# Kernel tuning notes

Hardware: AMD Instinct MI355X
Metric: run time of the kernel (lower is better)

## Reference

```python
import jax, jax.numpy as jnp
import numpy as np

# DeformConv3d hyperparams (from init_kwargs)
STRIDE = (1, 1, 1)
PAD = (1, 1, 1)
DIL = (1, 1, 1)
GROUPS = 1
DEFORM_GROUPS = 1  # reference assumes dg == 1


def setup_inputs() -> dict:
    key = jax.random.key(0)
    k1, k2, k3, k4 = jax.random.split(key, 4)
    x = jax.random.normal(k1, (2, 32, 24, 24, 24), jnp.float32)
    # offset channels = 3 * dg * kD*kH*kW = 81, layout [k_idx, (dz,dy,dx)]
    offset = jax.random.normal(k2, (2, 81, 24, 24, 24), jnp.float32)
    weight = jax.random.normal(k3, (64, 32, 3, 3, 3), jnp.float32) * 0.05
    bias = jax.random.normal(k4, (64,), jnp.float32) * 0.05
    return {"x": x, "offset": offset, "weight": weight, "bias": bias}


def _deform_conv3d(x, offset, weight, bias):
    B, C, D, H, W = x.shape
    Cout, Cg, kD, kH, kW = weight.shape
    sD, sH, sW = STRIDE
    pD, pH, pW = PAD
    dD, dH, dW = DIL
    Kn = kD * kH * kW
    Do = (D + 2 * pD - dD * (kD - 1) - 1) // sD + 1
    Ho = (H + 2 * pH - dH * (kH - 1) - 1) // sH + 1
    Wo = (W + 2 * pW - dW * (kW - 1) - 1) // sW + 1
    N = Do * Ho * Wo

    # offset: [B, Kn*3, Do,Ho,Wo] -> [B, Kn, 3, N]
    off = offset.reshape(B, Kn, 3, N)

    # kernel tap grid [Kn]
    kz, ky, kx = jnp.meshgrid(jnp.arange(kD), jnp.arange(kH), jnp.arange(kW), indexing='ij')
    kz, ky, kx = kz.reshape(Kn), ky.reshape(Kn), kx.reshape(Kn)
    # output grid [N]
    oz, oy, ox = jnp.meshgrid(jnp.arange(Do), jnp.arange(Ho), jnp.arange(Wo), indexing='ij')
    oz, oy, ox = oz.reshape(N), oy.reshape(N), ox.reshape(N)

    # sampling coords [B, Kn, N]
    z = (oz[None, None, :] * sD - pD) + kz[None, :, None] * dD + off[:, :, 0]
    y = (oy[None, None, :] * sH - pH) + ky[None, :, None] * dH + off[:, :, 1]
    xx = (ox[None, None, :] * sW - pW) + kx[None, :, None] * dW + off[:, :, 2]

    z0 = jnp.floor(z); fz = z - z0
    y0 = jnp.floor(y); fy = y - y0
    x0 = jnp.floor(xx); fx = xx - x0

    x_flat = x.reshape(B, C, D * H * W)
    acc = jnp.zeros((B, C, Kn * N), x.dtype)
    # 8 trilinear corners (fixed small loop)
    for dz in (0, 1):
        iz = z0 + dz
        wz = fz if dz else (1.0 - fz)
        for dy in (0, 1):
            iy = y0 + dy
            wy = fy if dy else (1.0 - fy)
            for dx in (0, 1):
                ix = x0 + dx
                wx = fx if dx else (1.0 - fx)
                valid = ((iz >= 0) & (iz < D) & (iy >= 0) & (iy < H)
                         & (ix >= 0) & (ix < W))
                w = (wz * wy * wx) * valid.astype(x.dtype)  # [B,Kn,N]
                izc = jnp.clip(iz, 0, D - 1).astype(jnp.int32)
                iyc = jnp.clip(iy, 0, H - 1).astype(jnp.int32)
                ixc = jnp.clip(ix, 0, W - 1).astype(jnp.int32)
                idx = (izc * H + iyc) * W + ixc  # [B,Kn,N]
                g = jnp.take_along_axis(x_flat, idx.reshape(B, 1, Kn * N), axis=2)
                acc = acc + g * w.reshape(B, 1, Kn * N)

    # im2col columns ordered (c, kz, ky, kx) to match weight layout
    cols = acc.reshape(B, C * Kn, N)
    Cpg = C // GROUPS
    Opg = Cout // GROUPS
    cols_g = cols.reshape(B, GROUPS, Cpg * Kn, N)
    w_g = weight.reshape(GROUPS, Opg, Cpg * Kn)
    out = jnp.einsum('gok,bgkn->bgon', w_g, cols_g).reshape(B, Cout, N)
    out = out + bias[None, :, None]
    return out.reshape(B, Cout, Do, Ho, Wo)


def reference(x, offset, weight, bias):
    return _deform_conv3d(x, offset, weight, bias)
```

## Files before the change

kernel.cpp:

```cpp
#include <hip/hip_runtime.h>
#include <hip/hip_fp16.h>


constexpr int B   = 2;
constexpr int C   = 32;
constexpr int D   = 24, H = 24, W = 24;
constexpr int CO  = 64;
constexpr int KN  = 27;
constexpr int DHW = D * H * W;
constexpr int N   = DHW;
constexpr int CK  = C * KN;

constexpr int TPB_MAIN = 256;
constexpr int NBLK     = (B * N) / 64;

constexpr int PREPX_BLKS = (B * DHW) / 256;
constexpr int PREPW_BLKS = (CO * CK) / 256;

using h8v   = __attribute__((ext_vector_type(8))) _Float16;
using f32x4 = __attribute__((ext_vector_type(4))) float;

__device__ __forceinline__ h8v splat8(float w) {
    const _Float16 h = (_Float16)w;
    h8v r;
    #pragma unroll
    for (int i = 0; i < 8; ++i) r[i] = h;
    return r;
}

__device__ __forceinline__ unsigned pack2h(float a, float b) {
    const _Float16 ha = (_Float16)a, hb = (_Float16)b;
    unsigned short ua, ub;
    __builtin_memcpy(&ua, &ha, 2);
    __builtin_memcpy(&ub, &hb, 2);
    return (unsigned)ua | ((unsigned)ub << 16);
}

__global__ __launch_bounds__(256)
void prep_fused(const float* __restrict__ x, const float* __restrict__ wgt,
                _Float16* __restrict__ xT, _Float16* __restrict__ wp) {
    const int bid = blockIdx.x;
    if (bid < PREPX_BLKS) {
        __shared__ unsigned s_t[256 * 21];
        const int tid = threadIdx.x;
        const int v0  = bid * 256;
        const int b   = (v0 >= DHW) ? 1 : 0;
        const int vox = (v0 - b * DHW) + tid;
        const float* xb = x + (size_t)(b * C) * DHW + vox;
        #pragma unroll
        for (int c2 = 0; c2 < 16; ++c2) {
            const float f0 = xb[(size_t)(2 * c2)     * DHW];
            const float f1 = xb[(size_t)(2 * c2 + 1) * DHW];
            s_t[tid * 21 + c2] = pack2h(f0, f1);
        }
        __syncthreads();
        unsigned r[16];
        #pragma unroll
        for (int j = 0; j < 16; ++j) r[j] = s_t[tid * 21 + j];
        int4* dst = reinterpret_cast<int4*>(xT + ((size_t)(v0 + tid)) * 32);
        dst[0] = make_int4(r[0],  r[1],  r[2],  r[3]);
        dst[1] = make_int4(r[4],  r[5],  r[6],  r[7]);
        dst[2] = make_int4(r[8],  r[9],  r[10], r[11]);
        dst[3] = make_int4(r[12], r[13], r[14], r[15]);
    } else {
        const int idx   = (bid - PREPX_BLKS) * 256 + threadIdx.x;
        const int j     = idx & 7;
        const int lane  = (idx >> 3) & 63;
        const int t     = idx >> 9;
        const int otile = t / 27;
        const int kstep = t - otile * 27;
        const int o     = otile * 16 + (lane & 15);
        const int c     = 8 * (lane >> 4) + j;
        wp[idx] = (_Float16)wgt[(size_t)o * CK + c * KN + kstep];
    }
}

__global__ __launch_bounds__(TPB_MAIN)
void deform_main(const float* __restrict__ off,
                 const _Float16* __restrict__ xT,
                 const _Float16* __restrict__ wp,
                 const float* __restrict__ bias,
                 float* __restrict__ out) {
    const int tid  = threadIdx.x;
    const int lane = tid & 63;
    const int wv   = tid >> 6;
    const int p    = lane & 15;
    const int q    = lane >> 4;

    const int gp = blockIdx.x * 64 + wv * 16 + p;
    const int b  = (gp >= N) ? 1 : 0;
    const int n  = gp - b * N;
    const int oz = n / 576;
    const int rr = n - oz * 576;
    const int oy = rr / 24;
    const int ox = rr - oy * 24;

    const float* offb  = off + (size_t)(b * 81) * N + n;
    const h8v*   xbase = reinterpret_cast<const h8v*>(xT) + (size_t)b * DHW * 4;
    const h8v*   wbase = reinterpret_cast<const h8v*>(wp);

    f32x4 acc[4];
    #pragma unroll
    for (int ot = 0; ot < 4; ++ot) acc[ot] = (f32x4){0.f, 0.f, 0.f, 0.f};

    #pragma unroll 1
    for (int ks = 0; ks < KN; ++ks) {
        const int kz = ks / 9;
        const int kr = ks - kz * 9;
        const int ky = kr / 3;
        const int kx = kr - ky * 3;

        const float offz = offb[(size_t)(ks * 3 + 0) * N];
        const float offy = offb[(size_t)(ks * 3 + 1) * N];
        const float offx = offb[(size_t)(ks * 3 + 2) * N];

        h8v afr[4];
        #pragma unroll
        for (int ot = 0; ot < 4; ++ot)
            afr[ot] = wbase[(ot * 27 + ks) * 64 + lane];

        const float z  = (float)(oz - 1 + kz) + offz;
        const float y  = (float)(oy - 1 + ky) + offy;
        const float xx = (float)(ox - 1 + kx) + offx;
        const float zf = floorf(z), yf = floorf(y), xf = floorf(xx);
        const float fz = z - zf, fy = y - yf, fx = xx - xf;
        const int z0 = (int)zf, y0 = (int)yf, x0 = (int)xf;

        int   cidx[8];
        float cw[8];
        #pragma unroll
        for (int cr = 0; cr < 8; ++cr) {
            const int cz = cr >> 2, cy = (cr >> 1) & 1, cx = cr & 1;
            const int iz = z0 + cz, iy = y0 + cy, ix = x0 + cx;
            const bool vd = ((unsigned)iz < (unsigned)D) &&
                            ((unsigned)iy < (unsigned)H) &&
                            ((unsigned)ix < (unsigned)W);
            const int izc = min(max(iz, 0), D - 1);
            const int iyc = min(max(iy, 0), H - 1);
            const int ixc = min(max(ix, 0), W - 1);
            cidx[cr] = (izc * H + iyc) * W + ixc;
            const float wz = cz ? fz : 1.0f - fz;
            const float wy = cy ? fy : 1.0f - fy;
            const float wx = cx ? fx : 1.0f - fx;
            cw[cr] = vd ? (wz * wy * wx) : 0.0f;
        }

        h8v v[8];
        #pragma unroll
        for (int cr = 0; cr < 8; ++cr)
            v[cr] = xbase[(size_t)cidx[cr] * 4 + q];

        h8v bfr = splat8(0.0f);
        #pragma unroll
        for (int cr = 0; cr < 8; ++cr)
            bfr += v[cr] * splat8(cw[cr]);

        #pragma unroll
        for (int ot = 0; ot < 4; ++ot)
            acc[ot] = __builtin_amdgcn_mfma_f32_16x16x32_f16(afr[ot], bfr,
                                                             acc[ot], 0, 0, 0);
    }

    #pragma unroll
    for (int ot = 0; ot < 4; ++ot) {
        #pragma unroll
        for (int r = 0; r < 4; ++r) {
            const int o = ot * 16 + q * 4 + r;
            out[((size_t)(b * CO + o)) * N + n] = acc[ot][r] + bias[o];
        }
    }
}

extern "C" void kernel_launch(void* const* d_in, const int* in_sizes, int n_in,
                              void* d_out, int out_size, void* d_ws, size_t ws_size,
                              hipStream_t stream) {
    const float* x    = (const float*)d_in[0];
    const float* off  = (const float*)d_in[1];
    const float* wgt  = (const float*)d_in[2];
    const float* bias = (const float*)d_in[3];
    float* out = (float*)d_out;

    _Float16* xT = (_Float16*)d_ws;
    _Float16* wp = (_Float16*)((char*)d_ws + 1769472);

    prep_fused<<<PREPX_BLKS + PREPW_BLKS, 256, 0, stream>>>(x, wgt, xT, wp);
    deform_main<<<NBLK, TPB_MAIN, 0, stream>>>(off, xT, wp, bias, out);
}
```

Measured before the change: 111.7 us.

## Split kernel taps across waves with LDS reduction and prefetch offsets

Each block now covers 16 output positions instead of 64, and its four waves each handle a subset of the 27 kernel taps (7/7/7/6). Partial MFMA accumulators are reduced through shared memory by wave 0, which writes the output. The per-tap offset loads are also software-prefetched one iteration ahead. This quadruples the block count and shortens each wave's serial gather chain to expose more parallelism and hide latency, at the cost of an LDS reduction, a barrier, and idle waves during the final store.

```diff
diff --git a/kernel.cpp b/kernel.cpp
--- a/kernel.cpp
+++ b/kernel.cpp
@@ -12,7 +12,7 @@
 constexpr int CK  = C * KN;
 
 constexpr int TPB_MAIN = 256;
-constexpr int NBLK     = (B * N) / 64;
+constexpr int NBLK     = (B * N) / 16;
 
 constexpr int PREPX_BLKS = (B * DHW) / 256;
 constexpr int PREPW_BLKS = (CO * CK) / 256;
@@ -81,13 +81,15 @@
                  const _Float16* __restrict__ wp,
                  const float* __restrict__ bias,
                  float* __restrict__ out) {
+    __shared__ float4 s_red[3 * 64 * 4];
+
     const int tid  = threadIdx.x;
     const int lane = tid & 63;
     const int wv   = tid >> 6;
     const int p    = lane & 15;
     const int q    = lane >> 4;
 
-    const int gp = blockIdx.x * 64 + wv * 16 + p;
+    const int gp = blockIdx.x * 16 + p;
     const int b  = (gp >= N) ? 1 : 0;
     const int n  = gp - b * N;
     const int oz = n / 576;
@@ -99,20 +101,28 @@
     const h8v*   xbase = reinterpret_cast<const h8v*>(xT) + (size_t)b * DHW * 4;
     const h8v*   wbase = reinterpret_cast<const h8v*>(wp);
 
+    const int k0 = wv * 7;
+    const int k1 = (wv == 3) ? 27 : (k0 + 7);
+
     f32x4 acc[4];
     #pragma unroll
     for (int ot = 0; ot < 4; ++ot) acc[ot] = (f32x4){0.f, 0.f, 0.f, 0.f};
 
+    float offz = offb[(size_t)(k0 * 3 + 0) * N];
+    float offy = offb[(size_t)(k0 * 3 + 1) * N];
+    float offx = offb[(size_t)(k0 * 3 + 2) * N];
+
     #pragma unroll 1
-    for (int ks = 0; ks < KN; ++ks) {
+    for (int ks = k0; ks < k1; ++ks) {
+        const int kn = (ks + 1 < k1) ? (ks + 1) : ks;
+        const float nfz = offb[(size_t)(kn * 3 + 0) * N];
+        const float nfy = offb[(size_t)(kn * 3 + 1) * N];
+        const float nfx = offb[(size_t)(kn * 3 + 2) * N];
+
         const int kz = ks / 9;
         const int kr = ks - kz * 9;
         const int ky = kr / 3;
         const int kx = kr - ky * 3;
-
-        const float offz = offb[(size_t)(ks * 3 + 0) * N];
-        const float offy = offb[(size_t)(ks * 3 + 1) * N];
-        const float offx = offb[(size_t)(ks * 3 + 2) * N];
 
         h8v afr[4];
         #pragma unroll
@@ -159,14 +169,36 @@
         for (int ot = 0; ot < 4; ++ot)
             acc[ot] = __builtin_amdgcn_mfma_f32_16x16x32_f16(afr[ot], bfr,
                                                              acc[ot], 0, 0, 0);
-    }
-
-    #pragma unroll
-    for (int ot = 0; ot < 4; ++ot) {
-        #pragma unroll
-        for (int r = 0; r < 4; ++r) {
-            const int o = ot * 16 + q * 4 + r;
-            out[((size_t)(b * CO + o)) * N + n] = acc[ot][r] + bias[o];
+
+        offz = nfz; offy = nfy; offx = nfx;
+    }
+
+    if (wv > 0) {
+        float4* dst = &s_red[((wv - 1) * 64 + lane) * 4];
+        #pragma unroll
+        for (int ot = 0; ot < 4; ++ot) {
+            dst[ot] = make_float4(acc[ot][0], acc[ot][1], acc[ot][2], acc[ot][3]);
+        }
+    }
+    __syncthreads();
+    if (wv == 0) {
+        #pragma unroll
+        for (int w = 0; w < 3; ++w) {
+            const float4* src = &s_red[(w * 64 + lane) * 4];
+            #pragma unroll
+            for (int ot = 0; ot < 4; ++ot) {
+                const float4 t = src[ot];
+                acc[ot][0] += t.x; acc[ot][1] += t.y;
+                acc[ot][2] += t.z; acc[ot][3] += t.w;
+            }
+        }
+        #pragma unroll
+        for (int ot = 0; ot < 4; ++ot) {
+            #pragma unroll
+            for (int r = 0; r < 4; ++r) {
+                const int o = ot * 16 + q * 4 + r;
+                out[((size_t)(b * CO + o)) * N + n] = acc[ot][r] + bias[o];
+            }
         }
     }
 }
```

After: 107.2 us. 4.0% less time.

## Stage a haloed 3D input tile in LDS for deformable trilinear gathers

Applied to the files above, without the earlier changes.

Each block now covers a 4x4x4 output cube and first loads a 10x10x10 halo (margin 3) of the fp16 channel-last input into shared memory, with a rotated channel-chunk swizzle to spread LDS bank accesses. The 8 corner gathers read from LDS whenever the sampled cell lies inside the halo and fall back to global loads otherwise. The aim is to replace scattered global gathers with LDS reads and reuse neighbouring voxels. In exchange it adds a cooperative load plus a barrier, uses 64KB of LDS per block, which limits occupancy, and leaves divergent paths for offsets that fall outside the halo.

```diff
diff --git a/kernel.cpp b/kernel.cpp
--- a/kernel.cpp
+++ b/kernel.cpp
@@ -11,8 +11,12 @@
 constexpr int N   = DHW;
 constexpr int CK  = C * KN;
 
+constexpr int LD   = 10;
+constexpr int MB   = 3;
+constexpr int NVOX = LD * LD * LD;
+
 constexpr int TPB_MAIN = 256;
-constexpr int NBLK     = (B * N) / 64;
+constexpr int NBLK     = B * 6 * 6 * 6;
 
 constexpr int PREPX_BLKS = (B * DHW) / 256;
 constexpr int PREPW_BLKS = (CO * CK) / 256;
@@ -75,28 +79,55 @@
     }
 }
 
+__device__ __forceinline__ int clamp0(int v, int hi) {
+    return min(max(v, 0), hi);
+}
+
 __global__ __launch_bounds__(TPB_MAIN)
 void deform_main(const float* __restrict__ off,
                  const _Float16* __restrict__ xT,
                  const _Float16* __restrict__ wp,
                  const float* __restrict__ bias,
                  float* __restrict__ out) {
+    __shared__ h8v s_x[NVOX * 4];
+
     const int tid  = threadIdx.x;
     const int lane = tid & 63;
     const int wv   = tid >> 6;
     const int p    = lane & 15;
     const int q    = lane >> 4;
 
-    const int gp = blockIdx.x * 64 + wv * 16 + p;
-    const int b  = (gp >= N) ? 1 : 0;
-    const int n  = gp - b * N;
-    const int oz = n / 576;
-    const int rr = n - oz * 576;
-    const int oy = rr / 24;
-    const int ox = rr - oy * 24;
-
-    const float* offb  = off + (size_t)(b * 81) * N + n;
-    const h8v*   xbase = reinterpret_cast<const h8v*>(xT) + (size_t)b * DHW * 4;
+    int t = blockIdx.x;
+    int b = 0;
+    if (t >= 216) { b = 1; t -= 216; }
+    const int tz = t / 36;
+    const int rt = t - tz * 36;
+    const int ty = rt / 6;
+    const int tx = rt - ty * 6;
+    const int oz0 = tz * 4, oy0 = ty * 4, ox0 = tx * 4;
+    const int tbz = oz0 - MB, tby = oy0 - MB, tbx = ox0 - MB;
+
+    const h8v* xbase = reinterpret_cast<const h8v*>(xT) + (size_t)b * DHW * 4;
+
+    for (int i = tid; i < NVOX * 4; i += TPB_MAIN) {
+        const int v  = i >> 2;
+        const int c  = i & 3;
+        const int vz = v / 100;
+        const int vr = v - vz * 100;
+        const int vy = vr / 10;
+        const int vx = vr - vy * 10;
+        const int gz = clamp0(tbz + vz, D - 1);
+        const int gy = clamp0(tby + vy, H - 1);
+        const int gx = clamp0(tbx + vx, W - 1);
+        const int gvox = (gz * H + gy) * W + gx;
+        s_x[v * 4 + ((c + v) & 3)] = xbase[(size_t)gvox * 4 + c];
+    }
+    __syncthreads();
+
+    const int pz = wv, py = p >> 2, px = p & 3;
+    const int oz = oz0 + pz, oy = oy0 + py, ox = ox0 + px;
+    const int n  = (oz * H + oy) * W + ox;
+    const float* offp  = off + (size_t)(b * 81) * N + n;
     const h8v*   wbase = reinterpret_cast<const h8v*>(wp);
 
     f32x4 acc[4];
@@ -110,9 +141,9 @@
         const int ky = kr / 3;
         const int kx = kr - ky * 3;
 
-        const float offz = offb[(size_t)(ks * 3 + 0) * N];
-        const float offy = offb[(size_t)(ks * 3 + 1) * N];
-        const float offx = offb[(size_t)(ks * 3 + 2) * N];
+        const float offz = offp[(size_t)(ks * 3 + 0) * N];
+        const float offy = offp[(size_t)(ks * 3 + 1) * N];
+        const float offx = offp[(size_t)(ks * 3 + 2) * N];
 
         h8v afr[4];
         #pragma unroll
@@ -126,7 +157,6 @@
         const float fz = z - zf, fy = y - yf, fx = xx - xf;
         const int z0 = (int)zf, y0 = (int)yf, x0 = (int)xf;
 
-        int   cidx[8];
         float cw[8];
         #pragma unroll
         for (int cr = 0; cr < 8; ++cr) {
@@ -135,25 +165,43 @@
             const bool vd = ((unsigned)iz < (unsigned)D) &&
                             ((unsigned)iy < (unsigned)H) &&
                             ((unsigned)ix < (unsigned)W);
-            const int izc = min(max(iz, 0), D - 1);
-            const int iyc = min(max(iy, 0), H - 1);
-            const int ixc = min(max(ix, 0), W - 1);
-            cidx[cr] = (izc * H + iyc) * W + ixc;
             const float wz = cz ? fz : 1.0f - fz;
             const float wy = cy ? fy : 1.0f - fy;
             const float wx = cx ? fx : 1.0f - fx;
             cw[cr] = vd ? (wz * wy * wx) : 0.0f;
         }
 
-        h8v v[8];
+        const int rz = z0 - tbz, ry = y0 - tby, rx = x0 - tbx;
+        const bool in = ((unsigned)rz < (unsigned)(LD - 1)) &&
+                        ((unsigned)ry < (unsigned)(LD - 1)) &&
+                        ((unsigned)rx < (unsigned)(LD - 1));
+
+        h8v v8[8];
+        if (in) {
+            const int rv0 = (rz * LD + ry) * LD + rx;
+            #pragma unroll
+            for (int cr = 0; cr < 8; ++cr) {
+                const int rv = rv0 + (cr >> 2) * 100 + ((cr >> 1) & 1) * 10
+                             + (cr & 1);
+                v8[cr] = s_x[rv * 4 + ((q + rv) & 3)];
+            }
+        }
+        if (!in) {
+            #pragma unroll
+            for (int cr = 0; cr < 8; ++cr) {
+                const int cz = cr >> 2, cy = (cr >> 1) & 1, cx = cr & 1;
+                const int izc = clamp0(z0 + cz, D - 1);
+                const int iyc = clamp0(y0 + cy, H - 1);
+                const int ixc = clamp0(x0 + cx, W - 1);
+                const int gvox = (izc * H + iyc) * W + ixc;
+                v8[cr] = xbase[(size_t)gvox * 4 + q];
+            }
+        }
+
+        h8v bfr = splat8(0.0f);
         #pragma unroll
         for (int cr = 0; cr < 8; ++cr)
-            v[cr] = xbase[(size_t)cidx[cr] * 4 + q];
-
-        h8v bfr = splat8(0.0f);
-        #pragma unroll
-        for (int cr = 0; cr < 8; ++cr)
-            bfr += v[cr] * splat8(cw[cr]);
+            bfr += v8[cr] * splat8(cw[cr]);
 
         #pragma unroll
         for (int ot = 0; ot < 4; ++ot)
```

New measurement: 104.7 us. 1.07x faster.
